# Kernel optimization log

Measured on AMD Instinct MI355X. Metric: run time of the kernel, lower is better.

## Reference

```python
import jax, jax.numpy as jnp
import numpy as np
from jax import lax

EPS = 1e-5

def silu(x):
    return x * jax.nn.sigmoid(x)

def setup_inputs() -> dict:
    key = jax.random.key(0)
    ks = jax.random.split(key, 8)
    B, T, H, W = 8, 32, 128, 128
    x = jax.random.normal(ks[0], (B, 1, T, H, W), jnp.float32)
    w_spatial = jax.random.normal(ks[1], (3, 1, 3, 3), jnp.float32) * 0.3
    b_spatial = jax.random.normal(ks[2], (3,), jnp.float32) * 0.1
    w_temporal = jax.random.normal(ks[3], (3, 1, 7, 1), jnp.float32) * 0.3
    b_temporal = jax.random.normal(ks[4], (3,), jnp.float32) * 0.1
    sn_weight = jnp.ones((1, 3, 1, 1, 1), jnp.float32)
    sn_bias = jnp.zeros((1, 3, 1, 1, 1), jnp.float32)
    mean_weight = jnp.ones((3,), jnp.float32)
    var_weight = jnp.ones((3,), jnp.float32)
    w_kv_s = jax.random.normal(ks[5], (2, T), jnp.float32) * (1.0 / np.sqrt(T))
    w_kv_t = jax.random.normal(ks[6], (2, H * W), jnp.float32) * (1.0 / np.sqrt(H * W))
    return dict(x=x, w_spatial=w_spatial, b_spatial=b_spatial,
                w_temporal=w_temporal, b_temporal=b_temporal,
                sn_weight=sn_weight, sn_bias=sn_bias,
                mean_weight=mean_weight, var_weight=var_weight,
                w_kv_s=w_kv_s, w_kv_t=w_kv_t)

def reference(x, w_spatial, b_spatial, w_temporal, b_temporal,
              sn_weight, sn_bias, mean_weight, var_weight, w_kv_s, w_kv_t):
    b, _, t, h, w = x.shape
    C = 3
    # --- spatial cone: timeIsHidden -> Conv2d(1,3,3,pad=1) -> SiLU ---
    xs = x.transpose(0, 2, 1, 3, 4).reshape(b * t, 1, h, w)  # (b t) c h w
    y = lax.conv_general_dilated(xs, w_spatial, (1, 1), ((1, 1), (1, 1)))
    y = silu(y + b_spatial[None, :, None, None])
    y = y.reshape(b, t, C, h, w).transpose(0, 2, 1, 3, 4)  # [b,3,t,h,w]
    # --- temporal cone: spaceIsHidden -> depthwise Conv2d(3,3,(7,1),groups=3) -> SiLU ---
    # kernel is (7,1) so convolving [b,3,t,hw] along t with width-1 in hw is identical math
    yt = y.reshape(b, C, t, h * w)
    z = lax.conv_general_dilated(yt, w_temporal, (1, 1), ((3, 3), (0, 0)),
                                 feature_group_count=C)
    z = silu(z + b_temporal[None, :, None, None]).reshape(b, C, t, h, w)
    # --- gain stage 1: SiLU + SwitchNorm3d(3) (training-mode statistics) ---
    g = silu(z)
    xr = g.reshape(b, C, -1)
    mean_in = xr.mean(-1, keepdims=True)              # [b,C,1] instance stats
    var_in = xr.var(-1, ddof=1, keepdims=True)        # torch .var is unbiased
    temp = var_in + mean_in ** 2
    mean_ln = mean_in.mean(1, keepdims=True)          # layer stats
    var_ln = temp.mean(1, keepdims=True) - mean_ln ** 2
    mean_bn = mean_in.mean(0, keepdims=True)          # batch stats
    var_bn = temp.mean(0, keepdims=True) - mean_bn ** 2
    mw = jax.nn.softmax(mean_weight)
    vw = jax.nn.softmax(var_weight)
    mean = mw[0] * mean_in + mw[1] * mean_ln + mw[2] * mean_bn
    var = vw[0] * var_in + vw[1] * var_ln + vw[2] * var_bn
    xn = ((xr - mean) / jnp.sqrt(var + EPS)).reshape(b, C, t, h, w)
    xn = xn * sn_weight + sn_bias
    # --- gain stage 2: GainControl (spatial/temporal kv via 1x1 convs) ---
    hw = h * w
    # to_kv_spatial: Conv2d(t,2,1,bias=False) over time-as-channel == contraction over t
    kv_s = jnp.einsum('bcthw,ot->bcohw', xn, w_kv_s)   # [b,C,2,h,w]
    ks_ = jax.nn.softmax(kv_s[:, :, 0].reshape(b, C, hw), axis=-1)[:, :, None, :]
    vs_ = kv_s[:, :, 1].reshape(b, C, hw)[:, :, None, :]
    # to_kv_temporal: Conv2d(hw,2,1,bias=False) over space-as-channel == contraction over hw
    xflat = xn.reshape(b, C, t, hw)
    kv_t = jnp.einsum('bcts,os->bcot', xflat, w_kv_t)  # [b,C,2,t]
    kt_ = jax.nn.softmax(kv_t[:, :, 0], axis=-1)[..., None]
    vt_ = kv_t[:, :, 1][..., None]
    out = jnp.sqrt(kt_ * ks_) * (vt_ * vs_)            # [b,C,t,hw]
    return out.reshape(b, C, t, h, w)
```

## Files before the change

### kernel.cpp

```cpp
#include <hip/hip_runtime.h>
#include <hip/hip_bf16.h>
#include <hip/hip_fp16.h>

#define Bn 8
#define Cn 3
#define Tn 32
#define Hn 128
#define Wn 128
#define HWn (Hn * Wn)
#define Nn (Tn * HWn)
#define EPSn 1e-5f
#define QT 2
#define SCH 128
#define SSW (SCH * QT)

__device__ __forceinline__ float silu_f(float v) {
    return v * __builtin_amdgcn_rcpf(1.0f + __expf(-v));
}

__global__ __launch_bounds__(256) void k1_spatial(
    const float* __restrict__ x, const float* __restrict__ wsp,
    const float* __restrict__ bsp, __half* __restrict__ y)
{
    const int tid = threadIdx.x, lane = tid & 63, wave = tid >> 6;
    const int bt = blockIdx.x;
    const int b = bt >> 5, t = bt & 31;
    const int row = blockIdx.y * 4 + wave;
    const int col = lane * 2;

    float w[27], bb[3];
#pragma unroll
    for (int i = 0; i < 27; ++i) w[i] = wsp[i];
#pragma unroll
    for (int i = 0; i < 3; ++i) bb[i] = bsp[i];

    const float* xsl = x + ((size_t)b * Tn + t) * HWn + (size_t)row * Wn + col;
    const bool upok = row > 0, dnok = row < Hn - 1;
    float2 xm = upok ? *(const float2*)(xsl - Wn) : make_float2(0.f, 0.f);
    float2 xc = *(const float2*)(xsl);
    float2 xp = dnok ? *(const float2*)(xsl + Wn) : make_float2(0.f, 0.f);
    float xv[3][4];
    {
        float lu, rd;
        lu = __shfl_up(xm.y, 1);  rd = __shfl_down(xm.x, 1);
        xv[0][0] = (lane == 0) ? 0.f : lu; xv[0][1] = xm.x; xv[0][2] = xm.y;
        xv[0][3] = (lane == 63) ? 0.f : rd;
        lu = __shfl_up(xc.y, 1);  rd = __shfl_down(xc.x, 1);
        xv[1][0] = (lane == 0) ? 0.f : lu; xv[1][1] = xc.x; xv[1][2] = xc.y;
        xv[1][3] = (lane == 63) ? 0.f : rd;
        lu = __shfl_up(xp.y, 1);  rd = __shfl_down(xp.x, 1);
        xv[2][0] = (lane == 0) ? 0.f : lu; xv[2][1] = xp.x; xv[2][2] = xp.y;
        xv[2][3] = (lane == 63) ? 0.f : rd;
    }
#pragma unroll
    for (int c = 0; c < 3; ++c) {
        float s0 = bb[c], s1 = bb[c];
#pragma unroll
        for (int i = 0; i < 3; ++i) {
#pragma unroll
            for (int j = 0; j < 3; ++j) {
                const float wv = w[c * 9 + i * 3 + j];
                s0 += wv * xv[i][j];
                s1 += wv * xv[i][j + 1];
            }
        }
        __half2 o = __floats2half2_rn(silu_f(s0), silu_f(s1));
        *(__half2*)(y + ((size_t)(b * 3 + c) * Tn + t) * HWn + (size_t)row * Wn + col) = o;
    }
}

template<int QTg>
__device__ __forceinline__ void k2_body(
    const __half* __restrict__ y, const float* __restrict__ wtp,
    const float* __restrict__ btp, const float* __restrict__ wkt,
    const float* __restrict__ wks,
    float* __restrict__ raw0, float* __restrict__ raw1,
    float* __restrict__ pt0p, float* __restrict__ pt1p,
    float* __restrict__ ss0p, float* __restrict__ ss1p)
{
    constexpr int O0 = QTg * 16;
    constexpr int O1 = O0 + 16;
    constexpr int SLO = (O0 - 3 < 0) ? 0 : (O0 - 3);
    constexpr int SHI = (O1 + 2 > Tn - 1) ? (Tn - 1) : (O1 + 2);

    const int tid = threadIdx.x, lane = tid & 63, wave = tid >> 6;
    const int sch = blockIdx.x * 2 + wave;
    const int bc  = blockIdx.y;
    const int c = bc % 3;
    const int s0i = sch * 128 + lane * 2;

    float wt_r[7];
#pragma unroll
    for (int i = 0; i < 7; ++i) wt_r[i] = wtp[c * 7 + i];
    const float bt_r = btp[c];

    const __half* yb = y + (size_t)bc * Nn + s0i;
    const float2 k0v = *(const float2*)(wkt + s0i);
    const float2 k1v = *(const float2*)(wkt + HWn + s0i);

    float2 ring[7];
    float2 a0 = make_float2(0.f, 0.f), a1 = make_float2(0.f, 0.f);
    float ps = 0.f, pq = 0.f;

#pragma unroll
    for (int tt = SLO; tt <= SHI + 3; ++tt) {
        if (tt <= SHI) {
            const __half2 hv = *(const __half2*)(yb + (size_t)tt * HWn);
            ring[tt % 7] = __half22float2(hv);
        }
        const int to = tt - 3;
        if (to >= O0 && to < O1) {
            float t0 = bt_r, t1 = bt_r;
#pragma unroll
            for (int k = 0; k < 7; ++k) {
                const int ts = to + k - 3;
                if (ts >= 0 && ts < Tn) {
                    const float wv = wt_r[k];
                    t0 += wv * ring[ts % 7].x;
                    t1 += wv * ring[ts % 7].y;
                }
            }
            const float g0 = silu_f(silu_f(t0));
            const float g1 = silu_f(silu_f(t1));
            const float wk0 = wks[to];
            const float wk1 = wks[Tn + to];
            a0.x += wk0 * g0; a0.y += wk0 * g1;
            a1.x += wk1 * g0; a1.y += wk1 * g1;
            ps += g0 + g1;
            pq += g0 * g0 + g1 * g1;
            float p0 = k0v.x * g0 + k0v.y * g1;
            float p1 = k1v.x * g0 + k1v.y * g1;
            p0 += __shfl_xor(p0, 1, 64); p0 += __shfl_xor(p0, 2, 64); p0 += __shfl_xor(p0, 4, 64);
            p1 += __shfl_xor(p1, 1, 64); p1 += __shfl_xor(p1, 2, 64); p1 += __shfl_xor(p1, 4, 64);
            float r = (lane & 1) ? p1 : p0;
            r += __shfl_xor(r, 8, 64);
            r += __shfl_xor(r, 16, 64);
            r += __shfl_xor(r, 32, 64);
            if (lane < 2) {
                float* dst = lane ? pt1p : pt0p;
                dst[((size_t)bc * Tn + to) * SCH + sch] = r;
            }
        }
    }

    {
        float p0 = ps, p1 = pq;
        p0 += __shfl_xor(p0, 1, 64); p0 += __shfl_xor(p0, 2, 64); p0 += __shfl_xor(p0, 4, 64);
        p1 += __shfl_xor(p1, 1, 64); p1 += __shfl_xor(p1, 2, 64); p1 += __shfl_xor(p1, 4, 64);
        float r = (lane & 1) ? p1 : p0;
        r += __shfl_xor(r, 8, 64);
        r += __shfl_xor(r, 16, 64);
        r += __shfl_xor(r, 32, 64);
        if (lane == 0) ss0p[(size_t)bc * SSW + sch * QT + QTg] = r;
        if (lane == 1) ss1p[(size_t)bc * SSW + sch * QT + QTg] = r;
    }
    {
        const size_t off = (size_t)(QTg * 24 + bc) * HWn + s0i;
        *(float2*)(raw0 + off) = a0;
        *(float2*)(raw1 + off) = a1;
    }
}

__global__ __launch_bounds__(128) void k2_temporal(
    const __half* __restrict__ y, const float* __restrict__ wtp,
    const float* __restrict__ btp, const float* __restrict__ wkt,
    const float* __restrict__ wks,
    float* __restrict__ raw0, float* __restrict__ raw1,
    float* __restrict__ pt0p, float* __restrict__ pt1p,
    float* __restrict__ ss0p, float* __restrict__ ss1p)
{
    if (blockIdx.z == 0)
        k2_body<0>(y, wtp, btp, wkt, wks, raw0, raw1, pt0p, pt1p, ss0p, ss1p);
    else
        k2_body<1>(y, wtp, btp, wkt, wks, raw0, raw1, pt0p, pt1p, ss0p, ss1p);
}

__global__ __launch_bounds__(256) void k3a_reduce(
    const float* __restrict__ pt0p, const float* __restrict__ pt1p,
    const float* __restrict__ ss0p, const float* __restrict__ ss1p,
    const float* __restrict__ wkt, const float* __restrict__ wks,
    float* __restrict__ kvt0r, float* __restrict__ kvt1r,
    float* __restrict__ ssS, float* __restrict__ ssSS, float* __restrict__ wsum)
{
    const int blk = blockIdx.x;
    const int tid = threadIdx.x;
    if (blk < Bn * Cn) {
        const int t = tid >> 3, g = tid & 7;
        const float4* p0 = (const float4*)(pt0p + ((size_t)blk * Tn + t) * SCH) + g * 4;
        const float4* p1 = (const float4*)(pt1p + ((size_t)blk * Tn + t) * SCH) + g * 4;
        float4 A0 = p0[0], A1 = p0[1], A2 = p0[2], A3 = p0[3];
        float4 B0 = p1[0], B1 = p1[1], B2 = p1[2], B3 = p1[3];
        float s0 = ((A0.x + A0.y) + (A0.z + A0.w)) + ((A1.x + A1.y) + (A1.z + A1.w))
                 + ((A2.x + A2.y) + (A2.z + A2.w)) + ((A3.x + A3.y) + (A3.z + A3.w));
        float s1 = ((B0.x + B0.y) + (B0.z + B0.w)) + ((B1.x + B1.y) + (B1.z + B1.w))
                 + ((B2.x + B2.y) + (B2.z + B2.w)) + ((B3.x + B3.y) + (B3.z + B3.w));
        s0 += __shfl_xor(s0, 1, 64); s0 += __shfl_xor(s0, 2, 64); s0 += __shfl_xor(s0, 4, 64);
        s1 += __shfl_xor(s1, 1, 64); s1 += __shfl_xor(s1, 2, 64); s1 += __shfl_xor(s1, 4, 64);
        if (g == 0) { kvt0r[blk * Tn + t] = s0; kvt1r[blk * Tn + t] = s1; }
        const float4* q0 = (const float4*)(ss0p + (size_t)blk * SSW);
        const float4* q1 = (const float4*)(ss1p + (size_t)blk * SSW);
        float a = 0.f, bb = 0.f;
        if (tid < SSW / 4) {
            float4 a4 = q0[tid], b4 = q1[tid];
            a = (a4.x + a4.y) + (a4.z + a4.w);
            bb = (b4.x + b4.y) + (b4.z + b4.w);
        }
        __shared__ float r0[256], r1[256];
        r0[tid] = a; r1[tid] = bb;
        __syncthreads();
        for (int off = 128; off > 0; off >>= 1) {
            if (tid < off) { r0[tid] += r0[tid + off]; r1[tid] += r1[tid + off]; }
            __syncthreads();
        }
        if (tid == 0) { ssS[blk] = r0[0]; ssSS[blk] = r1[0]; }
    } else {
        const float4* w0 = (const float4*)wkt;
        const float4* w1 = (const float4*)(wkt + HWn);
        float l0 = 0.f, l1 = 0.f;
        for (int i = tid; i < HWn / 4; i += 256) {
            float4 t0 = w0[i], t1 = w1[i];
            l0 += (t0.x + t0.y) + (t0.z + t0.w);
            l1 += (t1.x + t1.y) + (t1.z + t1.w);
        }
        __shared__ float r0[256], r1[256];
        r0[tid] = l0; r1[tid] = l1;
        __syncthreads();
        for (int off = 128; off > 0; off >>= 1) {
            if (tid < off) { r0[tid] += r0[tid + off]; r1[tid] += r1[tid + off]; }
            __syncthreads();
        }
        if (tid == 0) { wsum[0] = r0[0]; wsum[1] = r1[0]; }
        if (tid < 64) {
            float v = wks[tid];
            v += __shfl_xor(v, 1, 64); v += __shfl_xor(v, 2, 64);
            v += __shfl_xor(v, 4, 64); v += __shfl_xor(v, 8, 64);
            v += __shfl_xor(v, 16, 64);
            if (tid == 0) wsum[2] = v;
            if (tid == 32) wsum[3] = v;
        }
    }
}

__global__ __launch_bounds__(256) void k3b_finalize(
    const float* __restrict__ kvt0r, const float* __restrict__ kvt1r,
    const float* __restrict__ ssS, const float* __restrict__ ssSS,
    const float* __restrict__ mean_w, const float* __restrict__ var_w,
    const float* __restrict__ snw, const float* __restrict__ snb,
    const float* __restrict__ wsum,
    float* __restrict__ scale, float* __restrict__ shift, float* __restrict__ A)
{
    const int tid = threadIdx.x;
    __shared__ float kvt0[Bn * Cn * Tn], kvt1[Bn * Cn * Tn];
    __shared__ float sW[4];
    for (int i = tid; i < Bn * Cn * Tn; i += 256) { kvt0[i] = kvt0r[i]; kvt1[i] = kvt1r[i]; }
    if (tid < 4) sW[tid] = wsum[tid];
    __shared__ float sh_mean[24], sh_var[24], sh_temp[24];
    __shared__ float sh_mln[8], sh_vln[8], sh_mbn[3], sh_vbn[3];
    __shared__ float sh_mw[3], sh_vw[3];
    __shared__ float sh_scale[24], sh_shift[24];
    if (tid < 24) {
        float S = ssS[tid], SS = ssSS[tid];
        const float Nf = (float)Nn;
        float mean = S / Nf;
        float var = (SS - S * mean) / (Nf - 1.0f);
        sh_mean[tid] = mean; sh_var[tid] = var; sh_temp[tid] = var + mean * mean;
    }
    __syncthreads();
    if (tid == 0) {
        for (int b = 0; b < Bn; ++b) {
            float m = 0.f, tp = 0.f;
            for (int c = 0; c < Cn; ++c) { m += sh_mean[b * 3 + c]; tp += sh_temp[b * 3 + c]; }
            m *= (1.0f / 3.0f); tp *= (1.0f / 3.0f);
            sh_mln[b] = m; sh_vln[b] = tp - m * m;
        }
        for (int c = 0; c < Cn; ++c) {
            float m = 0.f, tp = 0.f;
            for (int b = 0; b < Bn; ++b) { m += sh_mean[b * 3 + c]; tp += sh_temp[b * 3 + c]; }
            m *= 0.125f; tp *= 0.125f;
            sh_mbn[c] = m; sh_vbn[c] = tp - m * m;
        }
        {
            float m0 = mean_w[0], m1 = mean_w[1], m2 = mean_w[2];
            float mm = fmaxf(m0, fmaxf(m1, m2));
            float e0 = __expf(m0 - mm), e1 = __expf(m1 - mm), e2 = __expf(m2 - mm);
            float inv = 1.0f / (e0 + e1 + e2);
            sh_mw[0] = e0 * inv; sh_mw[1] = e1 * inv; sh_mw[2] = e2 * inv;
        }
        {
            float v0 = var_w[0], v1 = var_w[1], v2 = var_w[2];
            float vm = fmaxf(v0, fmaxf(v1, v2));
            float e0 = __expf(v0 - vm), e1 = __expf(v1 - vm), e2 = __expf(v2 - vm);
            float inv = 1.0f / (e0 + e1 + e2);
            sh_vw[0] = e0 * inv; sh_vw[1] = e1 * inv; sh_vw[2] = e2 * inv;
        }
    }
    __syncthreads();
    if (tid < 24) {
        int b = tid / 3, c = tid % 3;
        float mean = sh_mw[0] * sh_mean[tid] + sh_mw[1] * sh_mln[b] + sh_mw[2] * sh_mbn[c];
        float var  = sh_vw[0] * sh_var[tid]  + sh_vw[1] * sh_vln[b] + sh_vw[2] * sh_vbn[c];
        float inv = 1.0f / sqrtf(var + EPSn);
        float sc = inv * snw[c];
        float sf = snb[c] - mean * sc;
        sh_scale[tid] = sc; sh_shift[tid] = sf;
        scale[tid] = sc; shift[tid] = sf;
    }
    __syncthreads();
    for (int i = tid; i < Bn * Cn * Tn; i += 256) {
        int bc = i >> 5;
        kvt0[i] = sh_scale[bc] * kvt0[i] + sh_shift[bc] * sW[0];
        kvt1[i] = sh_scale[bc] * kvt1[i] + sh_shift[bc] * sW[1];
    }
    __syncthreads();
    if (tid < 24) {
        float m = -3.4e38f;
        for (int t = 0; t < Tn; ++t) m = fmaxf(m, kvt0[tid * Tn + t]);
        float se = 0.f;
        for (int t = 0; t < Tn; ++t) se += __expf(kvt0[tid * Tn + t] - m);
        float inv = 1.0f / se;
        for (int t = 0; t < Tn; ++t)
            A[tid * Tn + t] = sqrtf(__expf(kvt0[tid * Tn + t] - m) * inv) * kvt1[tid * Tn + t];
    }
}

__global__ __launch_bounds__(256) void k5a_maxsum(
    const float* __restrict__ raw0, const float* __restrict__ raw1,
    const float* __restrict__ scale, const float* __restrict__ shift,
    const float* __restrict__ wsum, float* __restrict__ v0s,
    float* __restrict__ v1s, float2* __restrict__ ms)
{
    const int ch = blockIdx.x;
    const int bc = blockIdx.y;
    const int tid = threadIdx.x, lane = tid & 63, wave = tid >> 6;
    const float sc = scale[bc], sf = shift[bc];
    const float c0 = sf * wsum[2], c1 = sf * wsum[3];
    const size_t idx = (size_t)bc * HWn + ch * 2048 + tid * 8;
    float4 r0a = make_float4(0.f, 0.f, 0.f, 0.f), r0b = r0a, r1a = r0a, r1b = r0a;
#pragma unroll
    for (int q = 0; q < QT; ++q) {
        const float* p0 = raw0 + (size_t)q * 24 * HWn + idx;
        const float* p1 = raw1 + (size_t)q * 24 * HWn + idx;
        float4 t0 = ((const float4*)p0)[0], t1 = ((const float4*)p0)[1];
        float4 u0 = ((const float4*)p1)[0], u1 = ((const float4*)p1)[1];
        r0a.x += t0.x; r0a.y += t0.y; r0a.z += t0.z; r0a.w += t0.w;
        r0b.x += t1.x; r0b.y += t1.y; r0b.z += t1.z; r0b.w += t1.w;
        r1a.x += u0.x; r1a.y += u0.y; r1a.z += u0.z; r1a.w += u0.w;
        r1b.x += u1.x; r1b.y += u1.y; r1b.z += u1.z; r1b.w += u1.w;
    }
    float v0[8] = { sc * r0a.x + c0, sc * r0a.y + c0, sc * r0a.z + c0, sc * r0a.w + c0,
                    sc * r0b.x + c0, sc * r0b.y + c0, sc * r0b.z + c0, sc * r0b.w + c0 };
    float v1[8] = { sc * r1a.x + c1, sc * r1a.y + c1, sc * r1a.z + c1, sc * r1a.w + c1,
                    sc * r1b.x + c1, sc * r1b.y + c1, sc * r1b.z + c1, sc * r1b.w + c1 };
    ((float4*)(v0s + idx))[0] = make_float4(v0[0], v0[1], v0[2], v0[3]);
    ((float4*)(v0s + idx))[1] = make_float4(v0[4], v0[5], v0[6], v0[7]);
    ((float4*)(v1s + idx))[0] = make_float4(v1[0], v1[1], v1[2], v1[3]);
    ((float4*)(v1s + idx))[1] = make_float4(v1[4], v1[5], v1[6], v1[7]);
    float m = -3.4e38f;
#pragma unroll
    for (int i = 0; i < 8; ++i) m = fmaxf(m, v0[i]);
#pragma unroll
    for (int d = 1; d < 64; d <<= 1) m = fmaxf(m, __shfl_xor(m, d, 64));
    __shared__ float wm[4], wsm[4];
    if (lane == 0) wm[wave] = m;
    __syncthreads();
    const float M = fmaxf(fmaxf(wm[0], wm[1]), fmaxf(wm[2], wm[3]));
    float s = 0.f;
#pragma unroll
    for (int i = 0; i < 8; ++i) s += __expf(v0[i] - M);
#pragma unroll
    for (int d = 1; d < 64; d <<= 1) s += __shfl_xor(s, d, 64);
    if (lane == 0) wsm[wave] = s;
    __syncthreads();
    if (tid == 0) {
        float2 o; o.x = M; o.y = wsm[0] + wsm[1] + wsm[2] + wsm[3];
        ms[bc * 8 + ch] = o;
    }
}

__global__ __launch_bounds__(256) void k6_outer(
    const float* __restrict__ v0s, const float* __restrict__ v1s,
    const float2* __restrict__ ms, const float* __restrict__ A,
    float* __restrict__ out)
{
    const int ch = blockIdx.x;
    const int bc = blockIdx.y;
    const int tid = threadIdx.x;
    __shared__ float a[Tn];
    if (tid < Tn) a[tid] = A[bc * Tn + tid];
    float M = -3.4e38f;
#pragma unroll
    for (int j = 0; j < 8; ++j) M = fmaxf(M, ms[bc * 8 + j].x);
    float S = 0.f;
#pragma unroll
    for (int j = 0; j < 8; ++j) S += ms[bc * 8 + j].y * __expf(ms[bc * 8 + j].x - M);
    const float invS = __builtin_amdgcn_rcpf(S);
    const int s = ch * 1024 + tid * 4;
    float4 r0 = *(const float4*)(v0s + (size_t)bc * HWn + s);
    float4 r1 = *(const float4*)(v1s + (size_t)bc * HWn + s);
    float4 Bv;
    Bv.x = sqrtf(__expf(r0.x - M) * invS) * r1.x;
    Bv.y = sqrtf(__expf(r0.y - M) * invS) * r1.y;
    Bv.z = sqrtf(__expf(r0.z - M) * invS) * r1.z;
    Bv.w = sqrtf(__expf(r0.w - M) * invS) * r1.w;
    __syncthreads();
    float* op = out + (size_t)bc * Nn + s;
#pragma unroll
    for (int t = 0; t < Tn; ++t) {
        const float av = a[t];
        float4 o; o.x = av * Bv.x; o.y = av * Bv.y; o.z = av * Bv.z; o.w = av * Bv.w;
        *(float4*)(op + (size_t)t * HWn) = o;
    }
}

extern "C" void kernel_launch(void* const* d_in, const int* in_sizes, int n_in,
                              void* d_out, int out_size, void* d_ws, size_t ws_size,
                              hipStream_t stream) {
    const float* x          = (const float*)d_in[0];
    const float* w_spatial  = (const float*)d_in[1];
    const float* b_spatial  = (const float*)d_in[2];
    const float* w_temporal = (const float*)d_in[3];
    const float* b_temporal = (const float*)d_in[4];
    const float* sn_weight  = (const float*)d_in[5];
    const float* sn_bias    = (const float*)d_in[6];
    const float* mean_weight= (const float*)d_in[7];
    const float* var_weight = (const float*)d_in[8];
    const float* w_kv_s     = (const float*)d_in[9];
    const float* w_kv_t     = (const float*)d_in[10];
    float* out = (float*)d_out;
    float* ws  = (float*)d_ws;

    __half* yh   = (__half*)ws;
    float* raw0  = ws + 6291456;
    float* raw1  = raw0 + (size_t)QT * Bn * Cn * HWn;
    float* pt0p  = raw1 + (size_t)QT * Bn * Cn * HWn;
    float* pt1p  = pt0p + (size_t)Bn * Cn * Tn * SCH;
    float* ss0p  = pt1p + (size_t)Bn * Cn * Tn * SCH;
    float* ss1p  = ss0p + (size_t)Bn * Cn * SSW;
    float* v0s   = ss1p + (size_t)Bn * Cn * SSW;
    float* v1s   = v0s + (size_t)Bn * Cn * HWn;
    float* kvt0r = v1s + (size_t)Bn * Cn * HWn;
    float* kvt1r = kvt0r + Bn * Cn * Tn;
    float* ssS   = kvt1r + Bn * Cn * Tn;
    float* ssSS  = ssS + 24;
    float* scale = ssSS + 24;
    float* shift = scale + 24;
    float* A     = shift + 24;
    float* wsum  = A + Bn * Cn * Tn;
    float2* ms   = (float2*)(wsum + 4);

    k1_spatial<<<dim3(Bn * Tn, Hn / 4), 256, 0, stream>>>(x, w_spatial, b_spatial, yh);
    k2_temporal<<<dim3(SCH / 2, Bn * Cn, QT), 128, 0, stream>>>(yh, w_temporal,
                                                                b_temporal, w_kv_t,
                                                                w_kv_s, raw0, raw1,
                                                                pt0p, pt1p, ss0p, ss1p);
    k3a_reduce<<<Bn * Cn + 1, 256, 0, stream>>>(pt0p, pt1p, ss0p, ss1p, w_kv_t, w_kv_s,
                                                kvt0r, kvt1r, ssS, ssSS, wsum);
    k3b_finalize<<<1, 256, 0, stream>>>(kvt0r, kvt1r, ssS, ssSS,
                                        mean_weight, var_weight, sn_weight, sn_bias,
                                        wsum, scale, shift, A);
    k5a_maxsum<<<dim3(8, Bn * Cn), 256, 0, stream>>>(raw0, raw1, scale, shift, wsum,
                                                     v0s, v1s, ms);
    k6_outer<<<dim3(16, Bn * Cn), 256, 0, stream>>>(v0s, v1s, ms, A, out);
}
```

Baseline: 66.39 us.

## Fuse finalize, softmax stats and outer product into one kernel; widen spatial conv

Merges the three trailing kernels (stat finalization, spatial-softmax max/sum, outer-product write) into a single kernel. Each block recomputes the SwitchNorm scale/shift and the temporal softmax factor redundantly, and recomputes the spatial softmax max and sum over its whole HW plane. This removes two launches and the v0s/v1s/ms intermediates, at the cost of each of the 16 blocks per channel rereading raw0 twice. The spatial conv kernel now computes 4 outputs per thread with float4 loads, and 32-lane groups each handle one row.

```diff
diff --git a/kernel.cpp b/kernel.cpp
--- a/kernel.cpp
+++ b/kernel.cpp
@@ -22,11 +22,12 @@
     const float* __restrict__ x, const float* __restrict__ wsp,
     const float* __restrict__ bsp, __half* __restrict__ y)
 {
-    const int tid = threadIdx.x, lane = tid & 63, wave = tid >> 6;
+    const int tid = threadIdx.x;
+    const int sub = tid & 31;
     const int bt = blockIdx.x;
     const int b = bt >> 5, t = bt & 31;
-    const int row = blockIdx.y * 4 + wave;
-    const int col = lane * 2;
+    const int row = blockIdx.y * 8 + (tid >> 5);
+    const int col = sub * 4;
 
     float w[27], bb[3];
 #pragma unroll
@@ -36,25 +37,26 @@
 
     const float* xsl = x + ((size_t)b * Tn + t) * HWn + (size_t)row * Wn + col;
     const bool upok = row > 0, dnok = row < Hn - 1;
-    float2 xm = upok ? *(const float2*)(xsl - Wn) : make_float2(0.f, 0.f);
-    float2 xc = *(const float2*)(xsl);
-    float2 xp = dnok ? *(const float2*)(xsl + Wn) : make_float2(0.f, 0.f);
-    float xv[3][4];
+    const float4 z4 = make_float4(0.f, 0.f, 0.f, 0.f);
+    float4 xm = upok ? *(const float4*)(xsl - Wn) : z4;
+    float4 xc = *(const float4*)(xsl);
+    float4 xp = dnok ? *(const float4*)(xsl + Wn) : z4;
+    float xv[3][6];
     {
         float lu, rd;
-        lu = __shfl_up(xm.y, 1);  rd = __shfl_down(xm.x, 1);
-        xv[0][0] = (lane == 0) ? 0.f : lu; xv[0][1] = xm.x; xv[0][2] = xm.y;
-        xv[0][3] = (lane == 63) ? 0.f : rd;
-        lu = __shfl_up(xc.y, 1);  rd = __shfl_down(xc.x, 1);
-        xv[1][0] = (lane == 0) ? 0.f : lu; xv[1][1] = xc.x; xv[1][2] = xc.y;
-        xv[1][3] = (lane == 63) ? 0.f : rd;
-        lu = __shfl_up(xp.y, 1);  rd = __shfl_down(xp.x, 1);
-        xv[2][0] = (lane == 0) ? 0.f : lu; xv[2][1] = xp.x; xv[2][2] = xp.y;
-        xv[2][3] = (lane == 63) ? 0.f : rd;
+        lu = __shfl_up(xm.w, 1);  rd = __shfl_down(xm.x, 1);
+        xv[0][0] = (sub == 0) ? 0.f : lu; xv[0][1] = xm.x; xv[0][2] = xm.y;
+        xv[0][3] = xm.z; xv[0][4] = xm.w; xv[0][5] = (sub == 31) ? 0.f : rd;
+        lu = __shfl_up(xc.w, 1);  rd = __shfl_down(xc.x, 1);
+        xv[1][0] = (sub == 0) ? 0.f : lu; xv[1][1] = xc.x; xv[1][2] = xc.y;
+        xv[1][3] = xc.z; xv[1][4] = xc.w; xv[1][5] = (sub == 31) ? 0.f : rd;
+        lu = __shfl_up(xp.w, 1);  rd = __shfl_down(xp.x, 1);
+        xv[2][0] = (sub == 0) ? 0.f : lu; xv[2][1] = xp.x; xv[2][2] = xp.y;
+        xv[2][3] = xp.z; xv[2][4] = xp.w; xv[2][5] = (sub == 31) ? 0.f : rd;
     }
 #pragma unroll
     for (int c = 0; c < 3; ++c) {
-        float s0 = bb[c], s1 = bb[c];
+        float s0 = bb[c], s1 = bb[c], s2 = bb[c], s3 = bb[c];
 #pragma unroll
         for (int i = 0; i < 3; ++i) {
 #pragma unroll
@@ -62,10 +64,15 @@
                 const float wv = w[c * 9 + i * 3 + j];
                 s0 += wv * xv[i][j];
                 s1 += wv * xv[i][j + 1];
+                s2 += wv * xv[i][j + 2];
+                s3 += wv * xv[i][j + 3];
             }
         }
-        __half2 o = __floats2half2_rn(silu_f(s0), silu_f(s1));
-        *(__half2*)(y + ((size_t)(b * 3 + c) * Tn + t) * HWn + (size_t)row * Wn + col) = o;
+        __half2 o01 = __floats2half2_rn(silu_f(s0), silu_f(s1));
+        __half2 o23 = __floats2half2_rn(silu_f(s2), silu_f(s3));
+        __half2* dst = (__half2*)(y + ((size_t)(b * 3 + c) * Tn + t) * HWn
+                                  + (size_t)row * Wn + col);
+        dst[0] = o01; dst[1] = o23;
     }
 }
 
@@ -241,172 +248,127 @@
     }
 }
 
-__global__ __launch_bounds__(256) void k3b_finalize(
+__global__ __launch_bounds__(256) void k6_fused(
+    const float* __restrict__ raw0, const float* __restrict__ raw1,
     const float* __restrict__ kvt0r, const float* __restrict__ kvt1r,
     const float* __restrict__ ssS, const float* __restrict__ ssSS,
-    const float* __restrict__ mean_w, const float* __restrict__ var_w,
-    const float* __restrict__ snw, const float* __restrict__ snb,
-    const float* __restrict__ wsum,
-    float* __restrict__ scale, float* __restrict__ shift, float* __restrict__ A)
-{
-    const int tid = threadIdx.x;
-    __shared__ float kvt0[Bn * Cn * Tn], kvt1[Bn * Cn * Tn];
-    __shared__ float sW[4];
-    for (int i = tid; i < Bn * Cn * Tn; i += 256) { kvt0[i] = kvt0r[i]; kvt1[i] = kvt1r[i]; }
-    if (tid < 4) sW[tid] = wsum[tid];
-    __shared__ float sh_mean[24], sh_var[24], sh_temp[24];
-    __shared__ float sh_mln[8], sh_vln[8], sh_mbn[3], sh_vbn[3];
-    __shared__ float sh_mw[3], sh_vw[3];
-    __shared__ float sh_scale[24], sh_shift[24];
-    if (tid < 24) {
-        float S = ssS[tid], SS = ssSS[tid];
-        const float Nf = (float)Nn;
-        float mean = S / Nf;
-        float var = (SS - S * mean) / (Nf - 1.0f);
-        sh_mean[tid] = mean; sh_var[tid] = var; sh_temp[tid] = var + mean * mean;
-    }
-    __syncthreads();
-    if (tid == 0) {
-        for (int b = 0; b < Bn; ++b) {
-            float m = 0.f, tp = 0.f;
-            for (int c = 0; c < Cn; ++c) { m += sh_mean[b * 3 + c]; tp += sh_temp[b * 3 + c]; }
-            m *= (1.0f / 3.0f); tp *= (1.0f / 3.0f);
-            sh_mln[b] = m; sh_vln[b] = tp - m * m;
-        }
-        for (int c = 0; c < Cn; ++c) {
-            float m = 0.f, tp = 0.f;
-            for (int b = 0; b < Bn; ++b) { m += sh_mean[b * 3 + c]; tp += sh_temp[b * 3 + c]; }
-            m *= 0.125f; tp *= 0.125f;
-            sh_mbn[c] = m; sh_vbn[c] = tp - m * m;
-        }
-        {
-            float m0 = mean_w[0], m1 = mean_w[1], m2 = mean_w[2];
-            float mm = fmaxf(m0, fmaxf(m1, m2));
-            float e0 = __expf(m0 - mm), e1 = __expf(m1 - mm), e2 = __expf(m2 - mm);
-            float inv = 1.0f / (e0 + e1 + e2);
-            sh_mw[0] = e0 * inv; sh_mw[1] = e1 * inv; sh_mw[2] = e2 * inv;
-        }
-        {
-            float v0 = var_w[0], v1 = var_w[1], v2 = var_w[2];
-            float vm = fmaxf(v0, fmaxf(v1, v2));
-            float e0 = __expf(v0 - vm), e1 = __expf(v1 - vm), e2 = __expf(v2 - vm);
-            float inv = 1.0f / (e0 + e1 + e2);
-            sh_vw[0] = e0 * inv; sh_vw[1] = e1 * inv; sh_vw[2] = e2 * inv;
-        }
-    }
-    __syncthreads();
-    if (tid < 24) {
-        int b = tid / 3, c = tid % 3;
-        float mean = sh_mw[0] * sh_mean[tid] + sh_mw[1] * sh_mln[b] + sh_mw[2] * sh_mbn[c];
-        float var  = sh_vw[0] * sh_var[tid]  + sh_vw[1] * sh_vln[b] + sh_vw[2] * sh_vbn[c];
-        float inv = 1.0f / sqrtf(var + EPSn);
-        float sc = inv * snw[c];
-        float sf = snb[c] - mean * sc;
-        sh_scale[tid] = sc; sh_shift[tid] = sf;
-        scale[tid] = sc; shift[tid] = sf;
-    }
-    __syncthreads();
-    for (int i = tid; i < Bn * Cn * Tn; i += 256) {
-        int bc = i >> 5;
-        kvt0[i] = sh_scale[bc] * kvt0[i] + sh_shift[bc] * sW[0];
-        kvt1[i] = sh_scale[bc] * kvt1[i] + sh_shift[bc] * sW[1];
-    }
-    __syncthreads();
-    if (tid < 24) {
-        float m = -3.4e38f;
-        for (int t = 0; t < Tn; ++t) m = fmaxf(m, kvt0[tid * Tn + t]);
-        float se = 0.f;
-        for (int t = 0; t < Tn; ++t) se += __expf(kvt0[tid * Tn + t] - m);
-        float inv = 1.0f / se;
-        for (int t = 0; t < Tn; ++t)
-            A[tid * Tn + t] = sqrtf(__expf(kvt0[tid * Tn + t] - m) * inv) * kvt1[tid * Tn + t];
-    }
-}
-
-__global__ __launch_bounds__(256) void k5a_maxsum(
-    const float* __restrict__ raw0, const float* __restrict__ raw1,
-    const float* __restrict__ scale, const float* __restrict__ shift,
-    const float* __restrict__ wsum, float* __restrict__ v0s,
-    float* __restrict__ v1s, float2* __restrict__ ms)
+    const float* __restrict__ wsum, const float* __restrict__ mean_w,
+    const float* __restrict__ var_w, const float* __restrict__ snw,
+    const float* __restrict__ snb, float* __restrict__ out)
 {
     const int ch = blockIdx.x;
     const int bc = blockIdx.y;
     const int tid = threadIdx.x, lane = tid & 63, wave = tid >> 6;
-    const float sc = scale[bc], sf = shift[bc];
+    const int b = bc / 3, c = bc % 3;
+    const float Nf = (float)Nn;
+
+    float mln = 0.f, tln = 0.f;
+#pragma unroll
+    for (int cc = 0; cc < 3; ++cc) {
+        float S = ssS[b * 3 + cc], SS = ssSS[b * 3 + cc];
+        float m = S / Nf;
+        float v = (SS - S * m) / (Nf - 1.0f);
+        mln += m; tln += v + m * m;
+    }
+    mln *= (1.0f / 3.0f); tln *= (1.0f / 3.0f);
+    const float vln = tln - mln * mln;
+    float mbn = 0.f, tbn = 0.f;
+#pragma unroll
+    for (int bb2 = 0; bb2 < 8; ++bb2) {
+        float S = ssS[bb2 * 3 + c], SS = ssSS[bb2 * 3 + c];
+        float m = S / Nf;
+        float v = (SS - S * m) / (Nf - 1.0f);
+        mbn += m; tbn += v + m * m;
+    }
+    mbn *= 0.125f; tbn *= 0.125f;
+    const float vbn = tbn - mbn * mbn;
+    const float S_own = ssS[bc], SS_own = ssSS[bc];
+    const float mean_in = S_own / Nf;
+    const float var_in = (SS_own - S_own * mean_in) / (Nf - 1.0f);
+    float mw0, mw1, mw2, vw0, vw1, vw2;
+    {
+        float m0 = mean_w[0], m1 = mean_w[1], m2 = mean_w[2];
+        float mm = fmaxf(m0, fmaxf(m1, m2));
+        float e0 = __expf(m0 - mm), e1 = __expf(m1 - mm), e2 = __expf(m2 - mm);
+        float inv = 1.0f / (e0 + e1 + e2);
+        mw0 = e0 * inv; mw1 = e1 * inv; mw2 = e2 * inv;
+    }
+    {
+        float v0 = var_w[0], v1 = var_w[1], v2 = var_w[2];
+        float vm = fmaxf(v0, fmaxf(v1, v2));
+        float e0 = __expf(v0 - vm), e1 = __expf(v1 - vm), e2 = __expf(v2 - vm);
+        float inv = 1.0f / (e0 + e1 + e2);
+        vw0 = e0 * inv; vw1 = e1 * inv; vw2 = e2 * inv;
+    }
+    const float mean = mw0 * mean_in + mw1 * mln + mw2 * mbn;
+    const float var  = vw0 * var_in + vw1 * vln + vw2 * vbn;
+    const float sc = snw[c] / sqrtf(var + EPSn);
+    const float sf = snb[c] - mean * sc;
     const float c0 = sf * wsum[2], c1 = sf * wsum[3];
-    const size_t idx = (size_t)bc * HWn + ch * 2048 + tid * 8;
-    float4 r0a = make_float4(0.f, 0.f, 0.f, 0.f), r0b = r0a, r1a = r0a, r1b = r0a;
-#pragma unroll
-    for (int q = 0; q < QT; ++q) {
-        const float* p0 = raw0 + (size_t)q * 24 * HWn + idx;
-        const float* p1 = raw1 + (size_t)q * 24 * HWn + idx;
-        float4 t0 = ((const float4*)p0)[0], t1 = ((const float4*)p0)[1];
-        float4 u0 = ((const float4*)p1)[0], u1 = ((const float4*)p1)[1];
-        r0a.x += t0.x; r0a.y += t0.y; r0a.z += t0.z; r0a.w += t0.w;
-        r0b.x += t1.x; r0b.y += t1.y; r0b.z += t1.z; r0b.w += t1.w;
-        r1a.x += u0.x; r1a.y += u0.y; r1a.z += u0.z; r1a.w += u0.w;
-        r1b.x += u1.x; r1b.y += u1.y; r1b.z += u1.z; r1b.w += u1.w;
-    }
-    float v0[8] = { sc * r0a.x + c0, sc * r0a.y + c0, sc * r0a.z + c0, sc * r0a.w + c0,
-                    sc * r0b.x + c0, sc * r0b.y + c0, sc * r0b.z + c0, sc * r0b.w + c0 };
-    float v1[8] = { sc * r1a.x + c1, sc * r1a.y + c1, sc * r1a.z + c1, sc * r1a.w + c1,
-                    sc * r1b.x + c1, sc * r1b.y + c1, sc * r1b.z + c1, sc * r1b.w + c1 };
-    ((float4*)(v0s + idx))[0] = make_float4(v0[0], v0[1], v0[2], v0[3]);
-    ((float4*)(v0s + idx))[1] = make_float4(v0[4], v0[5], v0[6], v0[7]);
-    ((float4*)(v1s + idx))[0] = make_float4(v1[0], v1[1], v1[2], v1[3]);
-    ((float4*)(v1s + idx))[1] = make_float4(v1[4], v1[5], v1[6], v1[7]);
-    float m = -3.4e38f;
-#pragma unroll
-    for (int i = 0; i < 8; ++i) m = fmaxf(m, v0[i]);
-#pragma unroll
-    for (int d = 1; d < 64; d <<= 1) m = fmaxf(m, __shfl_xor(m, d, 64));
-    __shared__ float wm[4], wsm[4];
-    if (lane == 0) wm[wave] = m;
+    const float Wt0 = wsum[0], Wt1 = wsum[1];
+
+    __shared__ float aSh[Tn];
+    if (tid < Tn) {
+        float k0 = sc * kvt0r[bc * Tn + tid] + sf * Wt0;
+        float k1 = sc * kvt1r[bc * Tn + tid] + sf * Wt1;
+        float m = k0;
+#pragma unroll
+        for (int d = 1; d < 32; d <<= 1) m = fmaxf(m, __shfl_xor(m, d, 64));
+        float e = __expf(k0 - m);
+        float s = e;
+#pragma unroll
+        for (int d = 1; d < 32; d <<= 1) s += __shfl_xor(s, d, 64);
+        aSh[tid] = sqrtf(e / s) * k1;
+    }
+
+    const float* p0a = raw0 + (size_t)bc * HWn;
+    const float* p0b = p0a + (size_t)24 * HWn;
+    float mloc = -3.4e38f;
+#pragma unroll
+    for (int i = 0; i < 16; ++i) {
+        const int idx = tid * 4 + i * 1024;
+        float4 u = *(const float4*)(p0a + idx);
+        float4 v = *(const float4*)(p0b + idx);
+        mloc = fmaxf(mloc, fmaxf(fmaxf(sc * (u.x + v.x) + c0, sc * (u.y + v.y) + c0),
+                                 fmaxf(sc * (u.z + v.z) + c0, sc * (u.w + v.w) + c0)));
+    }
+#pragma unroll
+    for (int d = 1; d < 64; d <<= 1) mloc = fmaxf(mloc, __shfl_xor(mloc, d, 64));
+    __shared__ float wred[4];
+    if (lane == 0) wred[wave] = mloc;
     __syncthreads();
-    const float M = fmaxf(fmaxf(wm[0], wm[1]), fmaxf(wm[2], wm[3]));
-    float s = 0.f;
-#pragma unroll
-    for (int i = 0; i < 8; ++i) s += __expf(v0[i] - M);
-#pragma unroll
-    for (int d = 1; d < 64; d <<= 1) s += __shfl_xor(s, d, 64);
-    if (lane == 0) wsm[wave] = s;
+    const float M = fmaxf(fmaxf(wred[0], wred[1]), fmaxf(wred[2], wred[3]));
     __syncthreads();
-    if (tid == 0) {
-        float2 o; o.x = M; o.y = wsm[0] + wsm[1] + wsm[2] + wsm[3];
-        ms[bc * 8 + ch] = o;
-    }
-}
-
-__global__ __launch_bounds__(256) void k6_outer(
-    const float* __restrict__ v0s, const float* __restrict__ v1s,
-    const float2* __restrict__ ms, const float* __restrict__ A,
-    float* __restrict__ out)
-{
-    const int ch = blockIdx.x;
-    const int bc = blockIdx.y;
-    const int tid = threadIdx.x;
-    __shared__ float a[Tn];
-    if (tid < Tn) a[tid] = A[bc * Tn + tid];
-    float M = -3.4e38f;
-#pragma unroll
-    for (int j = 0; j < 8; ++j) M = fmaxf(M, ms[bc * 8 + j].x);
-    float S = 0.f;
-#pragma unroll
-    for (int j = 0; j < 8; ++j) S += ms[bc * 8 + j].y * __expf(ms[bc * 8 + j].x - M);
-    const float invS = __builtin_amdgcn_rcpf(S);
+    float sloc = 0.f;
+#pragma unroll
+    for (int i = 0; i < 16; ++i) {
+        const int idx = tid * 4 + i * 1024;
+        float4 u = *(const float4*)(p0a + idx);
+        float4 v = *(const float4*)(p0b + idx);
+        sloc += __expf(sc * (u.x + v.x) + c0 - M) + __expf(sc * (u.y + v.y) + c0 - M)
+              + __expf(sc * (u.z + v.z) + c0 - M) + __expf(sc * (u.w + v.w) + c0 - M);
+    }
+#pragma unroll
+    for (int d = 1; d < 64; d <<= 1) sloc += __shfl_xor(sloc, d, 64);
+    if (lane == 0) wred[wave] = sloc;
+    __syncthreads();
+    const float Sexp = (wred[0] + wred[1]) + (wred[2] + wred[3]);
+    const float invS = __builtin_amdgcn_rcpf(Sexp);
+
     const int s = ch * 1024 + tid * 4;
-    float4 r0 = *(const float4*)(v0s + (size_t)bc * HWn + s);
-    float4 r1 = *(const float4*)(v1s + (size_t)bc * HWn + s);
+    const float* p1a = raw1 + (size_t)bc * HWn;
+    const float* p1b = p1a + (size_t)24 * HWn;
+    float4 u0 = *(const float4*)(p0a + s), v0 = *(const float4*)(p0b + s);
+    float4 u1 = *(const float4*)(p1a + s), v1 = *(const float4*)(p1b + s);
     float4 Bv;
-    Bv.x = sqrtf(__expf(r0.x - M) * invS) * r1.x;
-    Bv.y = sqrtf(__expf(r0.y - M) * invS) * r1.y;
-    Bv.z = sqrtf(__expf(r0.z - M) * invS) * r1.z;
-    Bv.w = sqrtf(__expf(r0.w - M) * invS) * r1.w;
-    __syncthreads();
+    Bv.x = sqrtf(__expf(sc * (u0.x + v0.x) + c0 - M) * invS) * (sc * (u1.x + v1.x) + c1);
+    Bv.y = sqrtf(__expf(sc * (u0.y + v0.y) + c0 - M) * invS) * (sc * (u1.y + v1.y) + c1);
+    Bv.z = sqrtf(__expf(sc * (u0.z + v0.z) + c0 - M) * invS) * (sc * (u1.z + v1.z) + c1);
+    Bv.w = sqrtf(__expf(sc * (u0.w + v0.w) + c0 - M) * invS) * (sc * (u1.w + v1.w) + c1);
     float* op = out + (size_t)bc * Nn + s;
 #pragma unroll
     for (int t = 0; t < Tn; ++t) {
-        const float av = a[t];
+        const float av = aSh[t];
         float4 o; o.x = av * Bv.x; o.y = av * Bv.y; o.z = av * Bv.z; o.w = av * Bv.w;
         *(float4*)(op + (size_t)t * HWn) = o;
     }
@@ -436,29 +398,20 @@
     float* pt1p  = pt0p + (size_t)Bn * Cn * Tn * SCH;
     float* ss0p  = pt1p + (size_t)Bn * Cn * Tn * SCH;
     float* ss1p  = ss0p + (size_t)Bn * Cn * SSW;
-    float* v0s   = ss1p + (size_t)Bn * Cn * SSW;
-    float* v1s   = v0s + (size_t)Bn * Cn * HWn;
-    float* kvt0r = v1s + (size_t)Bn * Cn * HWn;
+    float* kvt0r = ss1p + (size_t)Bn * Cn * SSW;
     float* kvt1r = kvt0r + Bn * Cn * Tn;
     float* ssS   = kvt1r + Bn * Cn * Tn;
     float* ssSS  = ssS + 24;
-    float* scale = ssSS + 24;
-    float* shift = scale + 24;
-    float* A     = shift + 24;
-    float* wsum  = A + Bn * Cn * Tn;
-    float2* ms   = (float2*)(wsum + 4);
-
-    k1_spatial<<<dim3(Bn * Tn, Hn / 4), 256, 0, stream>>>(x, w_spatial, b_spatial, yh);
+    float* wsum  = ssSS + 24;
+
+    k1_spatial<<<dim3(Bn * Tn, Hn / 8), 256, 0, stream>>>(x, w_spatial, b_spatial, yh);
     k2_temporal<<<dim3(SCH / 2, Bn * Cn, QT), 128, 0, stream>>>(yh, w_temporal,
                                                                 b_temporal, w_kv_t,
                                                                 w_kv_s, raw0, raw1,
                                                                 pt0p, pt1p, ss0p, ss1p);
     k3a_reduce<<<Bn * Cn + 1, 256, 0, stream>>>(pt0p, pt1p, ss0p, ss1p, w_kv_t, w_kv_s,
                                                 kvt0r, kvt1r, ssS, ssSS, wsum);
-    k3b_finalize<<<1, 256, 0, stream>>>(kvt0r, kvt1r, ssS, ssSS,
-                                        mean_weight, var_weight, sn_weight, sn_bias,
-                                        wsum, scale, shift, A);
-    k5a_maxsum<<<dim3(8, Bn * Cn), 256, 0, stream>>>(raw0, raw1, scale, shift, wsum,
-                                                     v0s, v1s, ms);
-    k6_outer<<<dim3(16, Bn * Cn), 256, 0, stream>>>(v0s, v1s, ms, A, out);
-}
+    k6_fused<<<dim3(16, Bn * Cn), 256, 0, stream>>>(raw0, raw1, kvt0r, kvt1r,
+                                                    ssS, ssSS, wsum, mean_weight,
+                                                    var_weight, sn_weight, sn_bias, out);
+}
```

Measured after the change: 63.61 us. -4.2%, faster.
